# Kernel optimization log

Hardware: AMD Instinct MI355X
Metric: run time of the kernel (lower is better)

The kernel has to match this reference:

```python
import jax, jax.numpy as jnp
import numpy as np

N_SPOT, N_CITY, N_WORD = 20000, 2000, 20000
E_HAS, E_IN, E_DESC, E_RDESC = 100000, 100000, 400000, 400000
HID = 256


def setup_inputs() -> dict:
    key = jax.random.key(0)
    ks = jax.random.split(key, 48)

    def g(i, shape, s):
        return jax.random.normal(ks[i], shape, dtype=jnp.float32) * s

    inp = {}
    inp['x_spot'] = g(0, (N_SPOT, 2560), 0.5)
    inp['x_city'] = g(1, (N_CITY, 128), 0.5)
    inp['x_word'] = g(2, (N_WORD, 300), 0.5)
    inp['W_att'] = g(3, (4, 512, 128), 0.05)  # 4 heads, per_dim=128
    inp['q_att'] = g(4, (4, 128), 0.1)
    i = 5
    for n, d in [('w1_has_s', 128), ('w1_has_t', 512), ('w1_in_s', 512), ('w1_in_t', 128),
                 ('w1_desc_s', 300), ('w1_desc_t', 512), ('w1_rdesc_s', 512), ('w1_rdesc_t', 300)]:
        inp[n] = g(i, (d, HID), 0.05); i += 1
    for n in ['w2_has_s', 'w2_has_t', 'w2_in_s', 'w2_in_t', 'w2_desc_s', 'w2_desc_t', 'w2_rdesc_s', 'w2_rdesc_t']:
        inp[n] = g(i, (HID, HID), 0.05); i += 1
    for n in ['wl_spot', 'wl_city', 'wl_word']:
        inp[n] = g(i, (HID, 1), 0.05); i += 1
    for n in ['bl_spot', 'bl_city', 'bl_word']:
        inp[n] = jnp.zeros((1,), jnp.float32)
    for n, e, hi in [('e_has_src', E_HAS, N_CITY), ('e_has_tgt', E_HAS, N_SPOT),
                     ('e_in_src', E_IN, N_SPOT), ('e_in_tgt', E_IN, N_CITY),
                     ('e_desc_src', E_DESC, N_WORD), ('e_desc_tgt', E_DESC, N_SPOT),
                     ('e_rdesc_src', E_RDESC, N_SPOT), ('e_rdesc_tgt', E_RDESC, N_WORD)]:
        inp[n] = jax.random.randint(ks[i], (e,), 0, hi, dtype=jnp.int32); i += 1
    return inp


def _attention(x, W_att, q_att):
    # AttentionModule(input_dim=512, num_heads=4, split=5): (N, 2560) -> (N, 512)
    x = x.reshape(-1, 5, 512)
    xw = jnp.einsum('nsi,hio->hnso', x, W_att)                      # (4,N,5,128)
    a = jax.nn.leaky_relu(jnp.einsum('hnso,ho->hns', xw, q_att), 0.2)
    a = jax.nn.softmax(a, axis=2)                                   # softmax over split dim
    out = jnp.einsum('hnso,hns->hno', xw, a)                        # (4,N,128)
    return jnp.transpose(out, (1, 0, 2)).reshape(x.shape[0], 4 * 128)


def _scatter_mean(src, idx, n):
    s = jax.ops.segment_sum(src, idx, num_segments=n)
    c = jax.ops.segment_sum(jnp.ones((src.shape[0], 1), src.dtype), idx, num_segments=n)
    return s / jnp.maximum(c, 1.0)


def _edge(x_s, x_t, w_s, w_t, src, tgt):
    # per-edge-type linear, gather on source index, scatter-mean into targets
    msg = (x_s @ w_s)[src]
    return x_t @ w_t + _scatter_mean(msg, tgt, x_t.shape[0])


def _conv(xs, xc, xw, w, e):
    spot = _edge(xc, xs, w['has_s'], w['has_t'], e['has_src'], e['has_tgt']) \
         + _edge(xw, xs, w['desc_s'], w['desc_t'], e['desc_src'], e['desc_tgt'])
    city = _edge(xs, xc, w['in_s'], w['in_t'], e['in_src'], e['in_tgt'])
    word = _edge(xs, xw, w['rdesc_s'], w['rdesc_t'], e['rdesc_src'], e['rdesc_tgt'])
    # div[spot]=2, div[city]=div[word]=1; ReLU flag applies a second (idempotent) relu
    return jax.nn.relu(spot * 0.5), jax.nn.relu(city), jax.nn.relu(word)


def reference(x_spot, x_city, x_word, W_att, q_att,
              w1_has_s, w1_has_t, w1_in_s, w1_in_t, w1_desc_s, w1_desc_t, w1_rdesc_s, w1_rdesc_t,
              w2_has_s, w2_has_t, w2_in_s, w2_in_t, w2_desc_s, w2_desc_t, w2_rdesc_s, w2_rdesc_t,
              wl_spot, bl_spot, wl_city, bl_city, wl_word, bl_word,
              e_has_src, e_has_tgt, e_in_src, e_in_tgt, e_desc_src, e_desc_tgt, e_rdesc_src, e_rdesc_tgt):
    e = dict(has_src=e_has_src, has_tgt=e_has_tgt, in_src=e_in_src, in_tgt=e_in_tgt,
             desc_src=e_desc_src, desc_tgt=e_desc_tgt, rdesc_src=e_rdesc_src, rdesc_tgt=e_rdesc_tgt)
    w1 = dict(has_s=w1_has_s, has_t=w1_has_t, in_s=w1_in_s, in_t=w1_in_t,
              desc_s=w1_desc_s, desc_t=w1_desc_t, rdesc_s=w1_rdesc_s, rdesc_t=w1_rdesc_t)
    w2 = dict(has_s=w2_has_s, has_t=w2_has_t, in_s=w2_in_s, in_t=w2_in_t,
              desc_s=w2_desc_s, desc_t=w2_desc_t, rdesc_s=w2_rdesc_s, rdesc_t=w2_rdesc_t)
    xs = _attention(x_spot, W_att, q_att)  # multi=True path
    s1, c1, wd1 = _conv(xs, x_city, x_word, w1, e)
    s2, c2, wd2 = _conv(s1, c1, wd1, w2, e)
    out_spot = s2 @ wl_spot + bl_spot
    out_city = c2 @ wl_city + bl_city
    out_word = wd2 @ wl_word + bl_word
    # concat=True: mean over the two layer outputs per node type
    return ((s1 + s2) * 0.5, (c1 + c2) * 0.5, (wd1 + wd2) * 0.5, out_spot, out_city, out_word)
```

## Files before the change

### kernel.cpp

```cpp
#include <hip/hip_runtime.h>
#include <hip/hip_bf16.h>

#define HID 256
#define NSPOT 20000
#define NCITY 2000
#define NWORD 20000

typedef __attribute__((ext_vector_type(8))) short bhalf8;
typedef __attribute__((ext_vector_type(4))) float floatx4;

__device__ inline float bf2f(unsigned short u) {
    union { unsigned int i; float f; } v; v.i = (unsigned int)u << 16; return v.f;
}
__device__ inline unsigned short f2bf(float f) {
    __hip_bfloat16 b = __float2bfloat16(f);
    return *reinterpret_cast<unsigned short*>(&b);
}
__device__ inline float4 ld4(const float* p, size_t off) {
    return *reinterpret_cast<const float4*>(p + off);
}

__global__ void wq_kernel(const float* __restrict__ W, const float* __restrict__ q,
                          float* __restrict__ wq) {
    int idx = blockIdx.x * 256 + threadIdx.x;
// ... 36 lines not shown
            float v = al[tid][s];
            v = (v >= 0.f) ? v : 0.2f * v;
            z[s] = v; m = fmaxf(m, v);
        }
        float e[5]; float sum = 0.f;
        #pragma unroll
        for (int s = 0; s < 5; s++) { e[s] = __expf(z[s] - m); sum += e[s]; }
        float r = 1.f / sum;
        #pragma unroll
        for (int s = 0; s < 5; s++) al[tid][s] = e[s] * r;
    }
    __syncthreads();
    float a0 = al[wave][0], a1 = al[wave][1], a2 = al[wave][2], a3 = al[wave][3], a4 = al[wave][4];
    __hip_bfloat16* xo = xbar + ((size_t)wave * NSPOT + n) * 512;
    #pragma unroll
    for (int j = 0; j < 8; j++) {
        int i = lane + j * 64;
        float v = a0 * xl[i] + a1 * xl[512 + i] + a2 * xl[1024 + i] + a3 * xl[1536 + i] + a4 * xl[2048 + i];
        xo[i] = __float2bfloat16(v);
    }
}

#define KP 40
__global__ __launch_bounds__(256) void gemm_bf16(
    const __hip_bfloat16* __restrict__ A, int lda, long sA,
    const __hip_bfloat16* __restrict__ Bt, int ldb, long sB,
    float* __restrict__ C, int ldc,
    __hip_bfloat16* __restrict__ Cb, int ldcb, long sCb,
    int M, int N, int K) {
    __shared__ short As[128 * KP];
    __shared__ short Bs[128 * KP];
    int z = blockIdx.z;
    A += (size_t)z * sA;
    Bt += (size_t)z * sB;
    if (Cb) Cb += (size_t)z * sCb;
    int tid = threadIdx.x;
    int wave = tid >> 6, lane = tid & 63;
    int wr = wave & 1, wc = wave >> 1;
    int quad = lane >> 4, l16 = lane & 15;
    int rowbase = blockIdx.x * 128;
    int colbase = blockIdx.y * 128;
    int srow = tid >> 2;
    int skoff = (tid & 3) * 8;
    floatx4 acc[4][4];
    #pragma unroll
    for (int i = 0; i < 4; i++)
        #pragma unroll
        for (int j = 0; j < 4; j++)
            acc[i][j] = (floatx4){0.f, 0.f, 0.f, 0.f};

    for (int k0 = 0; k0 < K; k0 += 32) {
        #pragma unroll
        for (int i = 0; i < 2; i++) {
            int r = srow + i * 64;
            int gr = rowbase + r;
            int4 va = make_int4(0, 0, 0, 0);
            if (gr < M) va = *(const int4*)(A + (size_t)gr * lda + k0 + skoff);
            *(int4*)(As + r * KP + skoff) = va;
            int4 vb = *(const int4*)(Bt + (size_t)(colbase + r) * ldb + k0 + skoff);
            *(int4*)(Bs + r * KP + skoff) = vb;
        }
        __syncthreads();
        bhalf8 af[4], bfr[4];
        #pragma unroll
        for (int rt = 0; rt < 4; rt++)
            af[rt] = *(const bhalf8*)(As + (wr * 64 + rt * 16 + l16) * KP + quad * 8);
        #pragma unroll
        for (int ct = 0; ct < 4; ct++)
            bfr[ct] = *(const bhalf8*)(Bs + (wc * 64 + ct * 16 + l16) * KP + quad * 8);
        #pragma unroll
        for (int rt = 0; rt < 4; rt++)
            #pragma unroll
            for (int ct = 0; ct < 4; ct++)
                acc[rt][ct] = __builtin_amdgcn_mfma_f32_16x16x32_bf16(af[rt], bfr[ct], acc[rt][ct], 0, 0, 0);
        __syncthreads();
    }
    #pragma unroll
    for (int rt = 0; rt < 4; rt++) {
        #pragma unroll
        for (int r = 0; r < 4; r++) {
            int grow = rowbase + wr * 64 + rt * 16 + quad * 4 + r;
            if (grow < M) {
                #pragma unroll
                for (int ct = 0; ct < 4; ct++) {
                    int gcol = colbase + wc * 64 + ct * 16 + l16;
                    float v = acc[rt][ct][r];
                    if (C)  C[(size_t)grow * ldc + gcol] = v;
                    if (Cb) Cb[(size_t)grow * ldcb + gcol] = __float2bfloat16(v);
                }
            }
        }
    }
}

struct GemmDesc {
    const __hip_bfloat16* A;
    const __hip_bfloat16* Bt;
    float* C;
    __hip_bfloat16* Cb;
    int lda, ldb, ldc, ldcb, M, K;
};
struct GemmDesc8 { GemmDesc d[8]; };

__global__ __launch_bounds__(256) void gemm_bf16_grouped(GemmDesc8 descs) {
    GemmDesc g = descs.d[blockIdx.z];
    int rowbase = blockIdx.x * 128;
    if (rowbase >= g.M) return;
    __shared__ short As[128 * KP];
    __shared__ short Bs[128 * KP];
    int tid = threadIdx.x;
    int wave = tid >> 6, lane = tid & 63;
    int wr = wave & 1, wc = wave >> 1;
    int quad = lane >> 4, l16 = lane & 15;
    int colbase = blockIdx.y * 128;
    int srow = tid >> 2;
    int skoff = (tid & 3) * 8;
    floatx4 acc[4][4];
    #pragma unroll
    for (int i = 0; i < 4; i++)
        #pragma unroll
        for (int j = 0; j < 4; j++)
            acc[i][j] = (floatx4){0.f, 0.f, 0.f, 0.f};

    for (int k0 = 0; k0 < g.K; k0 += 32) {
        #pragma unroll
        for (int i = 0; i < 2; i++) {
            int r = srow + i * 64;
            int gr = rowbase + r;
            int4 va = make_int4(0, 0, 0, 0);
            if (gr < g.M) va = *(const int4*)(g.A + (size_t)gr * g.lda + k0 + skoff);
            *(int4*)(As + r * KP + skoff) = va;
            int4 vb = *(const int4*)(g.Bt + (size_t)(colbase + r) * g.ldb + k0 + skoff);
            *(int4*)(Bs + r * KP + skoff) = vb;
        }
        __syncthreads();
        bhalf8 af[4], bfr[4];
        #pragma unroll
        for (int rt = 0; rt < 4; rt++)
            af[rt] = *(const bhalf8*)(As + (wr * 64 + rt * 16 + l16) * KP + quad * 8);
        #pragma unroll
        for (int ct = 0; ct < 4; ct++)
            bfr[ct] = *(const bhalf8*)(Bs + (wc * 64 + ct * 16 + l16) * KP + quad * 8);
        #pragma unroll
        for (int rt = 0; rt < 4; rt++)
            #pragma unroll
            for (int ct = 0; ct < 4; ct++)
                acc[rt][ct] = __builtin_amdgcn_mfma_f32_16x16x32_bf16(af[rt], bfr[ct], acc[rt][ct], 0, 0, 0);
        __syncthreads();
    }
    #pragma unroll
    for (int rt = 0; rt < 4; rt++) {
        #pragma unroll
        for (int r = 0; r < 4; r++) {
            int grow = rowbase + wr * 64 + rt * 16 + quad * 4 + r;
            if (grow < g.M) {
                #pragma unroll
                for (int ct = 0; ct < 4; ct++) {
                    int gcol = colbase + wc * 64 + ct * 16 + l16;
                    float v = acc[rt][ct][r];
                    if (g.C)  g.C[(size_t)grow * g.ldc + gcol] = v;
                    if (g.Cb) g.Cb[(size_t)grow * g.ldcb + gcol] = __float2bfloat16(v);
                }
            }
        }
    }
}

struct TDesc { const float* in; __hip_bfloat16* out; int K; int N; int Kp; };
struct TDesc8 { TDesc d[8]; };
__global__ void transpose_cast_kernel(TDesc8 descs) {
    TDesc dsc = descs.d[blockIdx.z];
    __shared__ float tile[32][33];
    int k0 = blockIdx.x * 32, n0 = blockIdx.y * 32;
    if (k0 >= dsc.Kp || n0 >= dsc.N) return;
    int tn = threadIdx.x & 31, t8 = threadIdx.x >> 5;
    #pragma unroll
    for (int i = 0; i < 4; i++) {
        int k = k0 + t8 * 4 + i;
        float v = 0.f;
        if (k < dsc.K && n0 + tn < dsc.N) v = dsc.in[(size_t)k * dsc.N + n0 + tn];
        tile[t8 * 4 + i][tn] = v;
    }
    __syncthreads();
    int kk = threadIdx.x & 31, n8 = threadIdx.x >> 5;
    #pragma unroll
    for (int i = 0; i < 4; i++) {
        int n = n0 + n8 * 4 + i;
        int k = k0 + kk;
        if (n < dsc.N && k < dsc.Kp)
            dsc.out[(size_t)n * dsc.Kp + k] = __float2bfloat16(tile[kk][n8 * 4 + i]);
    }
}

__global__ void cast_kernel(const float* __restrict__ in, __hip_bfloat16* __restrict__ out, int n) {
    int i = blockIdx.x * 256 + threadIdx.x;
    if (i < n) out[i] = __float2bfloat16(in[i]);
}

__global__ void cast_pad_kernel(const float* __restrict__ in, __hip_bfloat16* __restrict__ out,
                                int rows, int K, int Kp) {
    int idx = blockIdx.x * 256 + threadIdx.x;
    if (idx >= rows * Kp) return;
    int r = idx / Kp, k = idx - r * Kp;
// ... 23 lines not shown
    for (int i = lo; i < hi; i++) s += dd.deg[i];
    part[tid] = s;
    __syncthreads();
    if (tid == 0) {
        int acc = 0;
        for (int i = 0; i < 256; i++) { partx[i] = acc; acc += part[i]; }
        partx[256] = acc;
    }
    __syncthreads();
    int acc = partx[tid];
    for (int i = lo; i < hi; i++) { dd.rp[i] = acc; dd.cur[i] = acc; acc += dd.deg[i]; }
    if (tid == 0) dd.rp[n] = partx[256];
}

__global__ void fill4_kernel(EdgeDesc4 ds) {
    EdgeDesc d = ds.d[blockIdx.y];
    int e = blockIdx.x * 256 + threadIdx.x;
    if (e >= d.E) return;
    int t = d.tgt[e];
    int pos = atomicAdd(&d.cur[t], 1);
    d.cs[pos] = d.src[e];
}

struct AggDesc { const __hip_bfloat16* msg; const int* rp; const int* cs; float* outm; };
struct AggDesc4 { AggDesc d[4]; int start1, start2, start3; };

__global__ __launch_bounds__(256) void agg4_kernel(AggDesc4 ds, int nrows) {
    int row = blockIdx.x * 4 + (threadIdx.x >> 6);
    if (row >= nrows) return;
    int lane = threadIdx.x & 63;
    int gi = (row >= ds.start1) + (row >= ds.start2) + (row >= ds.start3);
    int base = (gi == 0) ? 0 : (gi == 1) ? ds.start1 : (gi == 2) ? ds.start2 : ds.start3;
    AggDesc g = ds.d[gi];
    int t = row - base;
    int lo = g.rp[t], hi = g.rp[t + 1];
    float a0 = 0.f, a1 = 0.f, a2 = 0.f, a3 = 0.f;
    int doff = lane * 4;
    int i = lo;
    for (; i + 4 <= hi; i += 4) {
        int s0 = g.cs[i], s1 = g.cs[i + 1], s2 = g.cs[i + 2], s3 = g.cs[i + 3];
        ushort4 u0 = *(const ushort4*)(g.msg + (size_t)s0 * HID + doff);
        ushort4 u1 = *(const ushort4*)(g.msg + (size_t)s1 * HID + doff);
        ushort4 u2 = *(const ushort4*)(g.msg + (size_t)s2 * HID + doff);
        ushort4 u3 = *(const ushort4*)(g.msg + (size_t)s3 * HID + doff);
        a0 += (bf2f(u0.x) + bf2f(u1.x)) + (bf2f(u2.x) + bf2f(u3.x));
        a1 += (bf2f(u0.y) + bf2f(u1.y)) + (bf2f(u2.y) + bf2f(u3.y));
        a2 += (bf2f(u0.z) + bf2f(u1.z)) + (bf2f(u2.z) + bf2f(u3.z));
        a3 += (bf2f(u0.w) + bf2f(u1.w)) + (bf2f(u2.w) + bf2f(u3.w));
    }
    for (; i < hi; i++) {
        ushort4 u = *(const ushort4*)(g.msg + (size_t)g.cs[i] * HID + doff);
        a0 += bf2f(u.x); a1 += bf2f(u.y); a2 += bf2f(u.z); a3 += bf2f(u.w);
    }
    float inv = 1.f / fmaxf((float)(hi - lo), 1.f);
    float4 o = make_float4(a0 * inv, a1 * inv, a2 * inv, a3 * inv);
    *reinterpret_cast<float4*>(g.outm + (size_t)t * HID + doff) = o;
}

__global__ __launch_bounds__(256) void combine1v_kernel(
    const float* Sa, const float* Sb, const float* mH, const float* mD,
    float* s1, __hip_bfloat16* s1b,
    const float* Sc, const float* mI, float* c1, __hip_bfloat16* c1b,
    const float* Sw, const float* mR, float* wd1, __hip_bfloat16* wd1b) {
    int row = blockIdx.x * 4 + (threadIdx.x >> 6);
    if (row >= NSPOT + NCITY + NWORD) return;
    int lane = threadIdx.x & 63;
    float4 v; float* of; __hip_bfloat16* ob; size_t off;
    if (row < NSPOT) {
        off = (size_t)row * HID + lane * 4;
        float4 a = ld4(Sa, off), b = ld4(Sb, off), h = ld4(mH, off), d = ld4(mD, off);
        v = make_float4(fmaxf((a.x + b.x + h.x + d.x) * 0.5f, 0.f),
                        fmaxf((a.y + b.y + h.y + d.y) * 0.5f, 0.f),
                        fmaxf((a.z + b.z + h.z + d.z) * 0.5f, 0.f),
                        fmaxf((a.w + b.w + h.w + d.w) * 0.5f, 0.f));
        of = s1; ob = s1b;
    } else if (row < NSPOT + NCITY) {
        off = (size_t)(row - NSPOT) * HID + lane * 4;
        float4 a = ld4(Sc, off), m = ld4(mI, off);
        v = make_float4(fmaxf(a.x + m.x, 0.f), fmaxf(a.y + m.y, 0.f),
                        fmaxf(a.z + m.z, 0.f), fmaxf(a.w + m.w, 0.f));
        of = c1; ob = c1b;
    } else {
        off = (size_t)(row - NSPOT - NCITY) * HID + lane * 4;
        float4 a = ld4(Sw, off), m = ld4(mR, off);
        v = make_float4(fmaxf(a.x + m.x, 0.f), fmaxf(a.y + m.y, 0.f),
                        fmaxf(a.z + m.z, 0.f), fmaxf(a.w + m.w, 0.f));
        of = wd1; ob = wd1b;
    }
    *reinterpret_cast<float4*>(of + off) = v;
    ushort4 ub = make_ushort4(f2bf(v.x), f2bf(v.y), f2bf(v.z), f2bf(v.w));
    *reinterpret_cast<ushort4*>((unsigned short*)ob + off) = ub;
}

__global__ __launch_bounds__(256) void finale_kernel(
    const float* Sa, const float* Sb, const float* mH, const float* mD,
    const float* s1, float* out0, const float* wls, const float* bls, float* out3,
    const float* Sc, const float* mI, const float* c1, float* out1,
    const float* wlc, const float* blc, float* out4,
    const float* Sw, const float* mR, const float* wd1, float* out2,
    const float* wlw, const float* blw, float* out5) {
    int row = blockIdx.x * 4 + (threadIdx.x >> 6);
    if (row >= NSPOT + NCITY + NWORD) return;
    int lane = threadIdx.x & 63;
    float4 v, p; const float* wl; const float* bl; float* om; float* od;
    int r; size_t off;
    if (row < NSPOT) {
        r = row; off = (size_t)r * HID + lane * 4;
        float4 a = ld4(Sa, off), b = ld4(Sb, off), h = ld4(mH, off), d = ld4(mD, off);
        v = make_float4(fmaxf((a.x + b.x + h.x + d.x) * 0.5f, 0.f),
                        fmaxf((a.y + b.y + h.y + d.y) * 0.5f, 0.f),
                        fmaxf((a.z + b.z + h.z + d.z) * 0.5f, 0.f),
                        fmaxf((a.w + b.w + h.w + d.w) * 0.5f, 0.f));
        p = ld4(s1, off); wl = wls; bl = bls; om = out0; od = out3;
    } else if (row < NSPOT + NCITY) {
        r = row - NSPOT; off = (size_t)r * HID + lane * 4;
        float4 a = ld4(Sc, off), m = ld4(mI, off);
        v = make_float4(fmaxf(a.x + m.x, 0.f), fmaxf(a.y + m.y, 0.f),
                        fmaxf(a.z + m.z, 0.f), fmaxf(a.w + m.w, 0.f));
        p = ld4(c1, off); wl = wlc; bl = blc; om = out1; od = out4;
    } else {
        r = row - NSPOT - NCITY; off = (size_t)r * HID + lane * 4;
        float4 a = ld4(Sw, off), m = ld4(mR, off);
        v = make_float4(fmaxf(a.x + m.x, 0.f), fmaxf(a.y + m.y, 0.f),
                        fmaxf(a.z + m.z, 0.f), fmaxf(a.w + m.w, 0.f));
        p = ld4(wd1, off); wl = wlw; bl = blw; om = out2; od = out5;
    }
    float4 m4 = make_float4((p.x + v.x) * 0.5f, (p.y + v.y) * 0.5f,
                            (p.z + v.z) * 0.5f, (p.w + v.w) * 0.5f);
    *reinterpret_cast<float4*>(om + off) = m4;
    float4 w = *reinterpret_cast<const float4*>(wl + lane * 4);
    float s = v.x * w.x + v.y * w.y + v.z * w.z + v.w * w.w;
    #pragma unroll
    for (int o2 = 32; o2 > 0; o2 >>= 1) s += __shfl_down(s, o2, 64);
    if (lane == 0) od[r] = s + bl[0];
}

extern "C" void kernel_launch(void* const* d_in, const int* in_sizes, int n_in,
                              void* d_out, int out_size, void* d_ws, size_t ws_size,
                              hipStream_t stream) {
    const float* x_spot   = (const float*)d_in[0];
    const float* x_city   = (const float*)d_in[1];
    const float* x_word   = (const float*)d_in[2];
    const float* W_att    = (const float*)d_in[3];
    const float* q_att    = (const float*)d_in[4];
    const float* w1[8] = { (const float*)d_in[5], (const float*)d_in[6], (const float*)d_in[7],
                           (const float*)d_in[8], (const float*)d_in[9], (const float*)d_in[10],
                           (const float*)d_in[11], (const float*)d_in[12] };
    const float* w2[8] = { (const float*)d_in[13], (const float*)d_in[14], (const float*)d_in[15],
                           (const float*)d_in[16], (const float*)d_in[17], (const float*)d_in[18],
                           (const float*)d_in[19], (const float*)d_in[20] };
    const float* wl_spot = (const float*)d_in[21];
    const float* wl_city = (const float*)d_in[22];
    const float* wl_word = (const float*)d_in[23];
// ... 4 lines not shown
    const int* e_has_tgt   = (const int*)d_in[28];
    const int* e_in_src    = (const int*)d_in[29];
    const int* e_in_tgt    = (const int*)d_in[30];
    const int* e_desc_src  = (const int*)d_in[31];
    const int* e_desc_tgt  = (const int*)d_in[32];
    const int* e_rdesc_src = (const int*)d_in[33];
    const int* e_rdesc_tgt = (const int*)d_in[34];
    const int E_has   = in_sizes[27];
    const int E_in    = in_sizes[29];
    const int E_desc  = in_sizes[31];
    const int E_rdesc = in_sizes[33];

    float* out = (float*)d_out;
    float* wsf = (float*)d_ws;
    typedef __hip_bfloat16 bf;

    size_t o = 0;
    auto alloc = [&](size_t nfloats) { float* p = wsf + o; o += (nfloats + 15) & ~(size_t)15; return p; };
    float* wqb       = alloc(2048);
    bf* xs_bf        = (bf*)alloc((size_t)NSPOT * 512 / 2);
    bf* x_city_bf    = (bf*)alloc((size_t)NCITY * 128 / 2);
    bf* x_word_bf    = (bf*)alloc((size_t)NWORD * 320 / 2);
    bf* Wt_att       = (bf*)alloc((size_t)4 * 128 * 512 / 2);
    int K1[8]  = {128, 512, 512, 128, 300, 512, 512, 300};
    int Kp1[8] = {128, 512, 512, 128, 320, 512, 512, 320};
    bf* Wt1[8];
    for (int i = 0; i < 8; i++) Wt1[i] = (bf*)alloc((size_t)256 * Kp1[i] / 2);
    bf* Wt2[8];
    for (int i = 0; i < 8; i++) Wt2[i] = (bf*)alloc((size_t)256 * 256 / 2);
    float* Sa = alloc((size_t)NSPOT * HID);
    float* Sb = alloc((size_t)NSPOT * HID);
    float* Sc = alloc((size_t)NCITY * HID);
    float* Sw = alloc((size_t)NWORD * HID);
    float* m_has   = alloc((size_t)NSPOT * HID);
    float* m_desc  = alloc((size_t)NSPOT * HID);
    float* m_in    = alloc((size_t)NCITY * HID);
    float* m_rdesc = alloc((size_t)NWORD * HID);
    float* s1  = alloc((size_t)NSPOT * HID);
    float* c1  = alloc((size_t)NCITY * HID);
    float* wd1 = alloc((size_t)NWORD * HID);
    size_t regX = o;
    bf* xbar_bf = (bf*)(wsf + regX);
    size_t ox = regX;
    auto allocX = [&](size_t nfloats) { float* p = wsf + ox; ox += (nfloats + 15) & ~(size_t)15; return p; };
    bf* P_has_bf   = (bf*)allocX((size_t)NCITY * HID / 2);
    bf* P_in_bf    = (bf*)allocX((size_t)NSPOT * HID / 2);
    bf* P_desc_bf  = (bf*)allocX((size_t)NWORD * HID / 2);
    bf* P_rdesc_bf = (bf*)allocX((size_t)NSPOT * HID / 2);
    bf* s1b = (bf*)allocX((size_t)NSPOT * HID / 2);
    bf* c1b = (bf*)allocX((size_t)NCITY * HID / 2);
    bf* wd1b = (bf*)allocX((size_t)NWORD * HID / 2);
    o = regX + (size_t)4 * NSPOT * 512 / 2;
    int* wsi = (int*)(wsf + o);
    size_t io = 0;
    int* deg_has    = wsi + io; io += NSPOT;
    int* deg_desc   = wsi + io; io += NSPOT;
    int* deg_in     = wsi + io; io += NCITY;
    int* deg_rdesc  = wsi + io; io += NWORD;
    size_t deg_bytes = io * sizeof(int);
    int* rp_has     = wsi + io; io += NSPOT + 1;
    int* rp_desc    = wsi + io; io += NSPOT + 1;
    int* rp_in      = wsi + io; io += NCITY + 1;
    int* rp_rdesc   = wsi + io; io += NWORD + 1;
    int* cur_has    = wsi + io; io += NSPOT + 1;
    int* cur_desc   = wsi + io; io += NSPOT + 1;
    int* cur_in     = wsi + io; io += NCITY + 1;
    int* cur_rdesc  = wsi + io; io += NWORD + 1;
    int* cs_has     = wsi + io; io += E_has;
    int* cs_desc    = wsi + io; io += E_desc;
    int* cs_in      = wsi + io; io += E_in;
    int* cs_rdesc   = wsi + io; io += E_rdesc;
    (void)ws_size; (void)n_in; (void)out_size;

    {
        TDesc8 t{};
        for (int i = 0; i < 4; i++)
            t.d[i] = TDesc{ W_att + (size_t)i * 512 * 128, Wt_att + (size_t)i * 128 * 512, 512, 128, 512 };
        hipLaunchKernelGGL(transpose_cast_kernel, dim3(16, 4, 4), dim3(256), 0, stream, t);
    }
    {
        TDesc8 t{};
        for (int i = 0; i < 8; i++) t.d[i] = TDesc{ w1[i], Wt1[i], K1[i], 256, Kp1[i] };
        hipLaunchKernelGGL(transpose_cast_kernel, dim3(16, 8, 8), dim3(256), 0, stream, t);
    }
    {
        TDesc8 t{};
        for (int i = 0; i < 8; i++) t.d[i] = TDesc{ w2[i], Wt2[i], 256, 256, 256 };
        hipLaunchKernelGGL(transpose_cast_kernel, dim3(8, 8, 8), dim3(256), 0, stream, t);
    }
    hipLaunchKernelGGL(cast_kernel, dim3((NCITY * 128 + 255) / 256), dim3(256), 0, stream,
                       x_city, x_city_bf, NCITY * 128);
    hipLaunchKernelGGL(cast_pad_kernel, dim3((NWORD * 320 + 255) / 256), dim3(256), 0, stream,
                       x_word, x_word_bf, NWORD, 300, 320);

    EdgeDesc4 ed;
    ed.d[0] = EdgeDesc{ e_has_src,   e_has_tgt,   E_has,   NSPOT, deg_has,   rp_has,   cur_has,   cs_has };
    ed.d[1] = EdgeDesc{ e_desc_src,  e_desc_tgt,  E_desc,  NSPOT, deg_desc,  rp_desc,  cur_desc,  cs_desc };
    ed.d[2] = EdgeDesc{ e_in_src,    e_in_tgt,    E_in,    NCITY, deg_in,    rp_in,    cur_in,    cs_in };
    ed.d[3] = EdgeDesc{ e_rdesc_src, e_rdesc_tgt, E_rdesc, NWORD, deg_rdesc, rp_rdesc, cur_rdesc, cs_rdesc };
    int Emax = E_has;
    if (E_desc > Emax) Emax = E_desc;
    if (E_in > Emax) Emax = E_in;
    if (E_rdesc > Emax) Emax = E_rdesc;
    hipMemsetAsync((void*)deg_has, 0, deg_bytes, stream);
    hipLaunchKernelGGL(hist4_kernel, dim3((Emax + 255) / 256, 4), dim3(256), 0, stream, ed);
    hipLaunchKernelGGL(scan4_kernel, dim3(4), dim3(256), 0, stream, ed);
    hipLaunchKernelGGL(fill4_kernel, dim3((Emax + 255) / 256, 4), dim3(256), 0, stream, ed);

    hipLaunchKernelGGL(wq_kernel, dim3(8), dim3(256), 0, stream, W_att, q_att, wqb);
    hipLaunchKernelGGL(attn_kernel, dim3(NSPOT), dim3(256), 0, stream, x_spot, wqb, xbar_bf);
    {
        dim3 g((NSPOT + 127) / 128, 1, 4);
        hipLaunchKernelGGL(gemm_bf16, g, dim3(256), 0, stream,
                           xbar_bf, 512, (long)NSPOT * 512, Wt_att, 512, (long)128 * 512,
                           nullptr, 0, xs_bf, 512, 128, NSPOT, 128, 512);
    }

    int gx = (NSPOT + 127) / 128;

    {
        GemmDesc8 gd;
        gd.d[0] = GemmDesc{ x_city_bf, Wt1[0], nullptr, P_has_bf,   128, 128, 0, HID, NCITY, 128 };
        gd.d[1] = GemmDesc{ xs_bf,     Wt1[1], Sa,      nullptr,    512, 512, HID, 0, NSPOT, 512 };
        gd.d[2] = GemmDesc{ xs_bf,     Wt1[2], nullptr, P_in_bf,    512, 512, 0, HID, NSPOT, 512 };
        gd.d[3] = GemmDesc{ x_city_bf, Wt1[3], Sc,      nullptr,    128, 128, HID, 0, NCITY, 128 };
        gd.d[4] = GemmDesc{ x_word_bf, Wt1[4], nullptr, P_desc_bf,  320, 320, 0, HID, NWORD, 320 };
        gd.d[5] = GemmDesc{ xs_bf,     Wt1[5], Sb,      nullptr,    512, 512, HID, 0, NSPOT, 512 };
        gd.d[6] = GemmDesc{ xs_bf,     Wt1[6], nullptr, P_rdesc_bf, 512, 512, 0, HID, NSPOT, 512 };
        gd.d[7] = GemmDesc{ x_word_bf, Wt1[7], Sw,      nullptr,    320, 320, HID, 0, NWORD, 320 };
        hipLaunchKernelGGL(gemm_bf16_grouped, dim3(gx, 2, 8), dim3(256), 0, stream, gd);
    }

    AggDesc4 ag;
    ag.start1 = NSPOT; ag.start2 = 2 * NSPOT; ag.start3 = 2 * NSPOT + NCITY;
    int agg_rows = 2 * NSPOT + NCITY + NWORD;
    ag.d[0] = AggDesc{ P_has_bf,   rp_has,   cs_has,   m_has };
    ag.d[1] = AggDesc{ P_desc_bf,  rp_desc,  cs_desc,  m_desc };
    ag.d[2] = AggDesc{ P_in_bf,    rp_in,    cs_in,    m_in };
    ag.d[3] = AggDesc{ P_rdesc_bf, rp_rdesc, cs_rdesc, m_rdesc };
    hipLaunchKernelGGL(agg4_kernel, dim3((agg_rows + 3) / 4), dim3(256), 0, stream, ag, agg_rows);
    hipLaunchKernelGGL(combine1v_kernel, dim3((NSPOT + NCITY + NWORD) / 4), dim3(256), 0, stream,
                       Sa, Sb, m_has, m_desc, s1, s1b,
                       Sc, m_in, c1, c1b,
                       Sw, m_rdesc, wd1, wd1b);

    {
        GemmDesc8 gd;
        gd.d[0] = GemmDesc{ c1b,  Wt2[0], nullptr, P_has_bf,   HID, HID, 0, HID, NCITY, HID };
        gd.d[1] = GemmDesc{ s1b,  Wt2[1], Sa,      nullptr,    HID, HID, HID, 0, NSPOT, HID };
        gd.d[2] = GemmDesc{ s1b,  Wt2[2], nullptr, P_in_bf,    HID, HID, 0, HID, NSPOT, HID };
        gd.d[3] = GemmDesc{ c1b,  Wt2[3], Sc,      nullptr,    HID, HID, HID, 0, NCITY, HID };
        gd.d[4] = GemmDesc{ wd1b, Wt2[4], nullptr, P_desc_bf,  HID, HID, 0, HID, NWORD, HID };
        gd.d[5] = GemmDesc{ s1b,  Wt2[5], Sb,      nullptr,    HID, HID, HID, 0, NSPOT, HID };
        gd.d[6] = GemmDesc{ s1b,  Wt2[6], nullptr, P_rdesc_bf, HID, HID, 0, HID, NSPOT, HID };
        gd.d[7] = GemmDesc{ wd1b, Wt2[7], Sw,      nullptr,    HID, HID, HID, 0, NWORD, HID };
        hipLaunchKernelGGL(gemm_bf16_grouped, dim3(gx, 2, 8), dim3(256), 0, stream, gd);
    }

    hipLaunchKernelGGL(agg4_kernel, dim3((agg_rows + 3) / 4), dim3(256), 0, stream, ag, agg_rows);

    float* out0 = out;
    float* out1 = out + (size_t)NSPOT * HID;
    float* out2 = out1 + (size_t)NCITY * HID;
    float* out3 = out2 + (size_t)NWORD * HID;
    float* out4 = out3 + NSPOT;
    float* out5 = out4 + NCITY;
    hipLaunchKernelGGL(finale_kernel, dim3((NSPOT + NCITY + NWORD) / 4), dim3(256), 0, stream,
                       Sa, Sb, m_has, m_desc, s1, out0, wl_spot, bl_spot, out3,
                       Sc, m_in, c1, out1, wl_city, bl_city, out4,
                       Sw, m_rdesc, wd1, out2, wl_word, bl_word, out5);
}
```

Baseline: 960.8 us.

## Fuse segment-mean aggregation into combine kernels and merge shared spot self-weights

Removes the separate agg4 kernel and its fp32 mean buffers by computing segment means inline in the combine and finale kernels. The two spot-target self-transform weights (has_t and desc_t) are pre-summed during transpose, so one GEMM writes a single Ss instead of Sa and Sb. The attention GEMM is expressed through the grouped kernel, which gains an N bound check. This cuts fp32 intermediate traffic and one GEMM per layer. The fused kernels do more gather work per row, and pre-summing the weights before the bf16 cast changes rounding slightly.

```diff
diff --git a/kernel.cpp b/kernel.cpp
--- a/kernel.cpp
+++ b/kernel.cpp
@@ -82,26 +82,31 @@
 }
 
 #define KP 40
-__global__ __launch_bounds__(256) void gemm_bf16(
-    const __hip_bfloat16* __restrict__ A, int lda, long sA,
-    const __hip_bfloat16* __restrict__ Bt, int ldb, long sB,
-    float* __restrict__ C, int ldc,
-    __hip_bfloat16* __restrict__ Cb, int ldcb, long sCb,
-    int M, int N, int K) {
+struct GemmDesc {
+    const __hip_bfloat16* A;
+    const __hip_bfloat16* Bt;
+    float* C;
+    __hip_bfloat16* Cb;
+    int lda, ldb, ldc, ldcb, M, K, N;
+};
+struct GemmDesc8 { GemmDesc d[8]; };
+
+__global__ __launch_bounds__(256) void gemm_grouped(GemmDesc8 descs) {
+    GemmDesc g = descs.d[blockIdx.z];
+    int rowbase = blockIdx.x * 128;
+    int colbase = blockIdx.y * 128;
+    if (rowbase >= g.M || colbase >= g.N) return;
     __shared__ short As[128 * KP];
     __shared__ short Bs[128 * KP];
-    int z = blockIdx.z;
-    A += (size_t)z * sA;
-    Bt += (size_t)z * sB;
-    if (Cb) Cb += (size_t)z * sCb;
     int tid = threadIdx.x;
     int wave = tid >> 6, lane = tid & 63;
     int wr = wave & 1, wc = wave >> 1;
     int quad = lane >> 4, l16 = lane & 15;
-    int rowbase = blockIdx.x * 128;
-    int colbase = blockIdx.y * 128;
     int srow = tid >> 2;
     int skoff = (tid & 3) * 8;
+    const __hip_bfloat16* A = g.A;
+    const __hip_bfloat16* Bt = g.Bt;
+    int lda = g.lda, ldb = g.ldb, M = g.M, K = g.K;
     floatx4 acc[4][4];
     #pragma unroll
     for (int i = 0; i < 4; i++)
@@ -145,79 +150,6 @@
                 for (int ct = 0; ct < 4; ct++) {
                     int gcol = colbase + wc * 64 + ct * 16 + l16;
                     float v = acc[rt][ct][r];
-                    if (C)  C[(size_t)grow * ldc + gcol] = v;
-                    if (Cb) Cb[(size_t)grow * ldcb + gcol] = __float2bfloat16(v);
-                }
-            }
-        }
-    }
-}
-
-struct GemmDesc {
-    const __hip_bfloat16* A;
-    const __hip_bfloat16* Bt;
-    float* C;
-    __hip_bfloat16* Cb;
-    int lda, ldb, ldc, ldcb, M, K;
-};
-struct GemmDesc8 { GemmDesc d[8]; };
-
-__global__ __launch_bounds__(256) void gemm_bf16_grouped(GemmDesc8 descs) {
-    GemmDesc g = descs.d[blockIdx.z];
-    int rowbase = blockIdx.x * 128;
-    if (rowbase >= g.M) return;
-    __shared__ short As[128 * KP];
-    __shared__ short Bs[128 * KP];
-    int tid = threadIdx.x;
-    int wave = tid >> 6, lane = tid & 63;
-    int wr = wave & 1, wc = wave >> 1;
-    int quad = lane >> 4, l16 = lane & 15;
-    int colbase = blockIdx.y * 128;
-    int srow = tid >> 2;
-    int skoff = (tid & 3) * 8;
-    floatx4 acc[4][4];
-    #pragma unroll
-    for (int i = 0; i < 4; i++)
-        #pragma unroll
-        for (int j = 0; j < 4; j++)
-            acc[i][j] = (floatx4){0.f, 0.f, 0.f, 0.f};
-
-    for (int k0 = 0; k0 < g.K; k0 += 32) {
-        #pragma unroll
-        for (int i = 0; i < 2; i++) {
-            int r = srow + i * 64;
-            int gr = rowbase + r;
-            int4 va = make_int4(0, 0, 0, 0);
-            if (gr < g.M) va = *(const int4*)(g.A + (size_t)gr * g.lda + k0 + skoff);
-            *(int4*)(As + r * KP + skoff) = va;
-            int4 vb = *(const int4*)(g.Bt + (size_t)(colbase + r) * g.ldb + k0 + skoff);
-            *(int4*)(Bs + r * KP + skoff) = vb;
-        }
-        __syncthreads();
-        bhalf8 af[4], bfr[4];
-        #pragma unroll
-        for (int rt = 0; rt < 4; rt++)
-            af[rt] = *(const bhalf8*)(As + (wr * 64 + rt * 16 + l16) * KP + quad * 8);
-        #pragma unroll
-        for (int ct = 0; ct < 4; ct++)
-            bfr[ct] = *(const bhalf8*)(Bs + (wc * 64 + ct * 16 + l16) * KP + quad * 8);
-        #pragma unroll
-        for (int rt = 0; rt < 4; rt++)
-            #pragma unroll
-            for (int ct = 0; ct < 4; ct++)
-                acc[rt][ct] = __builtin_amdgcn_mfma_f32_16x16x32_bf16(af[rt], bfr[ct], acc[rt][ct], 0, 0, 0);
-        __syncthreads();
-    }
-    #pragma unroll
-    for (int rt = 0; rt < 4; rt++) {
-        #pragma unroll
-        for (int r = 0; r < 4; r++) {
-            int grow = rowbase + wr * 64 + rt * 16 + quad * 4 + r;
-            if (grow < g.M) {
-                #pragma unroll
-                for (int ct = 0; ct < 4; ct++) {
-                    int gcol = colbase + wc * 64 + ct * 16 + l16;
-                    float v = acc[rt][ct][r];
                     if (g.C)  g.C[(size_t)grow * g.ldc + gcol] = v;
                     if (g.Cb) g.Cb[(size_t)grow * g.ldcb + gcol] = __float2bfloat16(v);
                 }
@@ -226,7 +158,7 @@
     }
 }
 
-struct TDesc { const float* in; __hip_bfloat16* out; int K; int N; int Kp; };
+struct TDesc { const float* in; const float* in2; __hip_bfloat16* out; int K; int N; int Kp; };
 struct TDesc8 { TDesc d[8]; };
 __global__ void transpose_cast_kernel(TDesc8 descs) {
     TDesc dsc = descs.d[blockIdx.z];
@@ -238,7 +170,10 @@
     for (int i = 0; i < 4; i++) {
         int k = k0 + t8 * 4 + i;
         float v = 0.f;
-        if (k < dsc.K && n0 + tn < dsc.N) v = dsc.in[(size_t)k * dsc.N + n0 + tn];
+        if (k < dsc.K && n0 + tn < dsc.N) {
+            v = dsc.in[(size_t)k * dsc.N + n0 + tn];
+            if (dsc.in2) v += dsc.in2[(size_t)k * dsc.N + n0 + tn];
+        }
         tile[t8 * 4 + i][tn] = v;
     }
     __syncthreads();
@@ -308,69 +243,70 @@
     d.cs[pos] = d.src[e];
 }
 
-struct AggDesc { const __hip_bfloat16* msg; const int* rp; const int* cs; float* outm; };
-struct AggDesc4 { AggDesc d[4]; int start1, start2, start3; };
-
-__global__ __launch_bounds__(256) void agg4_kernel(AggDesc4 ds, int nrows) {
-    int row = blockIdx.x * 4 + (threadIdx.x >> 6);
-    if (row >= nrows) return;
-    int lane = threadIdx.x & 63;
-    int gi = (row >= ds.start1) + (row >= ds.start2) + (row >= ds.start3);
-    int base = (gi == 0) ? 0 : (gi == 1) ? ds.start1 : (gi == 2) ? ds.start2 : ds.start3;
-    AggDesc g = ds.d[gi];
-    int t = row - base;
-    int lo = g.rp[t], hi = g.rp[t + 1];
+__device__ inline float4 seg_mean(const __hip_bfloat16* __restrict__ msg,
+                                  const int* __restrict__ rp, const int* __restrict__ cs,
+                                  int t, int doff) {
+    int lo = rp[t], hi = rp[t + 1];
     float a0 = 0.f, a1 = 0.f, a2 = 0.f, a3 = 0.f;
-    int doff = lane * 4;
     int i = lo;
     for (; i + 4 <= hi; i += 4) {
-        int s0 = g.cs[i], s1 = g.cs[i + 1], s2 = g.cs[i + 2], s3 = g.cs[i + 3];
-        ushort4 u0 = *(const ushort4*)(g.msg + (size_t)s0 * HID + doff);
-        ushort4 u1 = *(const ushort4*)(g.msg + (size_t)s1 * HID + doff);
-        ushort4 u2 = *(const ushort4*)(g.msg + (size_t)s2 * HID + doff);
-        ushort4 u3 = *(const ushort4*)(g.msg + (size_t)s3 * HID + doff);
+        int s0 = cs[i], s1 = cs[i + 1], s2 = cs[i + 2], s3 = cs[i + 3];
+        ushort4 u0 = *(const ushort4*)(msg + (size_t)s0 * HID + doff);
+        ushort4 u1 = *(const ushort4*)(msg + (size_t)s1 * HID + doff);
+        ushort4 u2 = *(const ushort4*)(msg + (size_t)s2 * HID + doff);
+        ushort4 u3 = *(const ushort4*)(msg + (size_t)s3 * HID + doff);
         a0 += (bf2f(u0.x) + bf2f(u1.x)) + (bf2f(u2.x) + bf2f(u3.x));
         a1 += (bf2f(u0.y) + bf2f(u1.y)) + (bf2f(u2.y) + bf2f(u3.y));
         a2 += (bf2f(u0.z) + bf2f(u1.z)) + (bf2f(u2.z) + bf2f(u3.z));
         a3 += (bf2f(u0.w) + bf2f(u1.w)) + (bf2f(u2.w) + bf2f(u3.w));
     }
     for (; i < hi; i++) {
-        ushort4 u = *(const ushort4*)(g.msg + (size_t)g.cs[i] * HID + doff);
+        ushort4 u = *(const ushort4*)(msg + (size_t)cs[i] * HID + doff);
         a0 += bf2f(u.x); a1 += bf2f(u.y); a2 += bf2f(u.z); a3 += bf2f(u.w);
     }
     float inv = 1.f / fmaxf((float)(hi - lo), 1.f);
-    float4 o = make_float4(a0 * inv, a1 * inv, a2 * inv, a3 * inv);
-    *reinterpret_cast<float4*>(g.outm + (size_t)t * HID + doff) = o;
-}
-
-__global__ __launch_bounds__(256) void combine1v_kernel(
-    const float* Sa, const float* Sb, const float* mH, const float* mD,
-    float* s1, __hip_bfloat16* s1b,
-    const float* Sc, const float* mI, float* c1, __hip_bfloat16* c1b,
-    const float* Sw, const float* mR, float* wd1, __hip_bfloat16* wd1b) {
+    return make_float4(a0 * inv, a1 * inv, a2 * inv, a3 * inv);
+}
+
+__global__ __launch_bounds__(256) void fused_ac1_kernel(
+    const __hip_bfloat16* __restrict__ Phas,   const int* __restrict__ rp_has,   const int* __restrict__ cs_has,
+    const __hip_bfloat16* __restrict__ Pdesc,  const int* __restrict__ rp_desc,  const int* __restrict__ cs_desc,
+    const __hip_bfloat16* __restrict__ Pin,    const int* __restrict__ rp_in,    const int* __restrict__ cs_in,
+    const __hip_bfloat16* __restrict__ Prdesc, const int* __restrict__ rp_rdesc, const int* __restrict__ cs_rdesc,
+    const float* __restrict__ Ss, const float* __restrict__ Sc, const float* __restrict__ Sw,
+    float* __restrict__ s1, __hip_bfloat16* __restrict__ s1b,
+    float* __restrict__ c1, __hip_bfloat16* __restrict__ c1b,
+    float* __restrict__ wd1, __hip_bfloat16* __restrict__ wd1b) {
     int row = blockIdx.x * 4 + (threadIdx.x >> 6);
     if (row >= NSPOT + NCITY + NWORD) return;
     int lane = threadIdx.x & 63;
+    int doff = lane * 4;
     float4 v; float* of; __hip_bfloat16* ob; size_t off;
     if (row < NSPOT) {
-        off = (size_t)row * HID + lane * 4;
-        float4 a = ld4(Sa, off), b = ld4(Sb, off), h = ld4(mH, off), d = ld4(mD, off);
-        v = make_float4(fmaxf((a.x + b.x + h.x + d.x) * 0.5f, 0.f),
-                        fmaxf((a.y + b.y + h.y + d.y) * 0.5f, 0.f),
-                        fmaxf((a.z + b.z + h.z + d.z) * 0.5f, 0.f),
-                        fmaxf((a.w + b.w + h.w + d.w) * 0.5f, 0.f));
+        float4 mh = seg_mean(Phas, rp_has, cs_has, row, doff);
+        float4 md = seg_mean(Pdesc, rp_desc, cs_desc, row, doff);
+        off = (size_t)row * HID + doff;
+        float4 s = ld4(Ss, off);
+        v = make_float4(fmaxf((s.x + mh.x + md.x) * 0.5f, 0.f),
+                        fmaxf((s.y + mh.y + md.y) * 0.5f, 0.f),
+                        fmaxf((s.z + mh.z + md.z) * 0.5f, 0.f),
+                        fmaxf((s.w + mh.w + md.w) * 0.5f, 0.f));
         of = s1; ob = s1b;
     } else if (row < NSPOT + NCITY) {
-        off = (size_t)(row - NSPOT) * HID + lane * 4;
-        float4 a = ld4(Sc, off), m = ld4(mI, off);
-        v = make_float4(fmaxf(a.x + m.x, 0.f), fmaxf(a.y + m.y, 0.f),
-                        fmaxf(a.z + m.z, 0.f), fmaxf(a.w + m.w, 0.f));
+        int r = row - NSPOT;
+        float4 mi = seg_mean(Pin, rp_in, cs_in, r, doff);
+        off = (size_t)r * HID + doff;
+        float4 s = ld4(Sc, off);
+        v = make_float4(fmaxf(s.x + mi.x, 0.f), fmaxf(s.y + mi.y, 0.f),
+                        fmaxf(s.z + mi.z, 0.f), fmaxf(s.w + mi.w, 0.f));
         of = c1; ob = c1b;
     } else {
-        off = (size_t)(row - NSPOT - NCITY) * HID + lane * 4;
-        float4 a = ld4(Sw, off), m = ld4(mR, off);
-        v = make_float4(fmaxf(a.x + m.x, 0.f), fmaxf(a.y + m.y, 0.f),
-                        fmaxf(a.z + m.z, 0.f), fmaxf(a.w + m.w, 0.f));
+        int r = row - NSPOT - NCITY;
+        float4 mr = seg_mean(Prdesc, rp_rdesc, cs_rdesc, r, doff);
+        off = (size_t)r * HID + doff;
+        float4 s = ld4(Sw, off);
+        v = make_float4(fmaxf(s.x + mr.x, 0.f), fmaxf(s.y + mr.y, 0.f),
+                        fmaxf(s.z + mr.z, 0.f), fmaxf(s.w + mr.w, 0.f));
         of = wd1; ob = wd1b;
     }
     *reinterpret_cast<float4*>(of + off) = v;
@@ -378,43 +314,54 @@
     *reinterpret_cast<ushort4*>((unsigned short*)ob + off) = ub;
 }
 
-__global__ __launch_bounds__(256) void finale_kernel(
-    const float* Sa, const float* Sb, const float* mH, const float* mD,
-    const float* s1, float* out0, const float* wls, const float* bls, float* out3,
-    const float* Sc, const float* mI, const float* c1, float* out1,
-    const float* wlc, const float* blc, float* out4,
-    const float* Sw, const float* mR, const float* wd1, float* out2,
-    const float* wlw, const float* blw, float* out5) {
+__global__ __launch_bounds__(256) void fused_finale_kernel(
+    const __hip_bfloat16* __restrict__ Phas,   const int* __restrict__ rp_has,   const int* __restrict__ cs_has,
+    const __hip_bfloat16* __restrict__ Pdesc,  const int* __restrict__ rp_desc,  const int* __restrict__ cs_desc,
+    const __hip_bfloat16* __restrict__ Pin,    const int* __restrict__ rp_in,    const int* __restrict__ cs_in,
+    const __hip_bfloat16* __restrict__ Prdesc, const int* __restrict__ rp_rdesc, const int* __restrict__ cs_rdesc,
+    const float* __restrict__ Ss, const float* __restrict__ Sc, const float* __restrict__ Sw,
+    const float* __restrict__ s1, const float* __restrict__ c1, const float* __restrict__ wd1,
+    float* __restrict__ out0, const float* __restrict__ wls, const float* __restrict__ bls, float* __restrict__ out3,
+    float* __restrict__ out1, const float* __restrict__ wlc, const float* __restrict__ blc, float* __restrict__ out4,
+    float* __restrict__ out2, const float* __restrict__ wlw, const float* __restrict__ blw, float* __restrict__ out5) {
     int row = blockIdx.x * 4 + (threadIdx.x >> 6);
     if (row >= NSPOT + NCITY + NWORD) return;
     int lane = threadIdx.x & 63;
+    int doff = lane * 4;
     float4 v, p; const float* wl; const float* bl; float* om; float* od;
     int r; size_t off;
     if (row < NSPOT) {
-        r = row; off = (size_t)r * HID + lane * 4;
-        float4 a = ld4(Sa, off), b = ld4(Sb, off), h = ld4(mH, off), d = ld4(mD, off);
-        v = make_float4(fmaxf((a.x + b.x + h.x + d.x) * 0.5f, 0.f),
-                        fmaxf((a.y + b.y + h.y + d.y) * 0.5f, 0.f),
-                        fmaxf((a.z + b.z + h.z + d.z) * 0.5f, 0.f),
-                        fmaxf((a.w + b.w + h.w + d.w) * 0.5f, 0.f));
+        r = row;
+        float4 mh = seg_mean(Phas, rp_has, cs_has, r, doff);
+        float4 md = seg_mean(Pdesc, rp_desc, cs_desc, r, doff);
+        off = (size_t)r * HID + doff;
+        float4 s = ld4(Ss, off);
+        v = make_float4(fmaxf((s.x + mh.x + md.x) * 0.5f, 0.f),
+                        fmaxf((s.y + mh.y + md.y) * 0.5f, 0.f),
+                        fmaxf((s.z + mh.z + md.z) * 0.5f, 0.f),
+                        fmaxf((s.w + mh.w + md.w) * 0.5f, 0.f));
         p = ld4(s1, off); wl = wls; bl = bls; om = out0; od = out3;
     } else if (row < NSPOT + NCITY) {
-        r = row - NSPOT; off = (size_t)r * HID + lane * 4;
-        float4 a = ld4(Sc, off), m = ld4(mI, off);
-        v = make_float4(fmaxf(a.x + m.x, 0.f), fmaxf(a.y + m.y, 0.f),
-                        fmaxf(a.z + m.z, 0.f), fmaxf(a.w + m.w, 0.f));
+        r = row - NSPOT;
+        float4 mi = seg_mean(Pin, rp_in, cs_in, r, doff);
+        off = (size_t)r * HID + doff;
+        float4 s = ld4(Sc, off);
+        v = make_float4(fmaxf(s.x + mi.x, 0.f), fmaxf(s.y + mi.y, 0.f),
+                        fmaxf(s.z + mi.z, 0.f), fmaxf(s.w + mi.w, 0.f));
         p = ld4(c1, off); wl = wlc; bl = blc; om = out1; od = out4;
     } else {
-        r = row - NSPOT - NCITY; off = (size_t)r * HID + lane * 4;
-        float4 a = ld4(Sw, off), m = ld4(mR, off);
-        v = make_float4(fmaxf(a.x + m.x, 0.f), fmaxf(a.y + m.y, 0.f),
-                        fmaxf(a.z + m.z, 0.f), fmaxf(a.w + m.w, 0.f));
+        r = row - NSPOT - NCITY;
+        float4 mr = seg_mean(Prdesc, rp_rdesc, cs_rdesc, r, doff);
+        off = (size_t)r * HID + doff;
+        float4 s = ld4(Sw, off);
+        v = make_float4(fmaxf(s.x + mr.x, 0.f), fmaxf(s.y + mr.y, 0.f),
+                        fmaxf(s.z + mr.z, 0.f), fmaxf(s.w + mr.w, 0.f));
         p = ld4(wd1, off); wl = wlw; bl = blw; om = out2; od = out5;
     }
     float4 m4 = make_float4((p.x + v.x) * 0.5f, (p.y + v.y) * 0.5f,
                             (p.z + v.z) * 0.5f, (p.w + v.w) * 0.5f);
     *reinterpret_cast<float4*>(om + off) = m4;
-    float4 w = *reinterpret_cast<const float4*>(wl + lane * 4);
+    float4 w = *reinterpret_cast<const float4*>(wl + doff);
     float s = v.x * w.x + v.y * w.y + v.z * w.z + v.w * w.w;
     #pragma unroll
     for (int o2 = 32; o2 > 0; o2 >>= 1) s += __shfl_down(s, o2, 64);
@@ -465,20 +412,14 @@
     bf* x_city_bf    = (bf*)alloc((size_t)NCITY * 128 / 2);
     bf* x_word_bf    = (bf*)alloc((size_t)NWORD * 320 / 2);
     bf* Wt_att       = (bf*)alloc((size_t)4 * 128 * 512 / 2);
-    int K1[8]  = {128, 512, 512, 128, 300, 512, 512, 300};
-    int Kp1[8] = {128, 512, 512, 128, 320, 512, 512, 320};
-    bf* Wt1[8];
-    for (int i = 0; i < 8; i++) Wt1[i] = (bf*)alloc((size_t)256 * Kp1[i] / 2);
-    bf* Wt2[8];
-    for (int i = 0; i < 8; i++) Wt2[i] = (bf*)alloc((size_t)256 * 256 / 2);
-    float* Sa = alloc((size_t)NSPOT * HID);
-    float* Sb = alloc((size_t)NSPOT * HID);
+    int Kp1[7] = {128, 512, 512, 128, 320, 512, 320};
+    bf* Wt1[7];
+    for (int i = 0; i < 7; i++) Wt1[i] = (bf*)alloc((size_t)256 * Kp1[i] / 2);
+    bf* Wt2[7];
+    for (int i = 0; i < 7; i++) Wt2[i] = (bf*)alloc((size_t)256 * 256 / 2);
+    float* Ss = alloc((size_t)NSPOT * HID);
     float* Sc = alloc((size_t)NCITY * HID);
     float* Sw = alloc((size_t)NWORD * HID);
-    float* m_has   = alloc((size_t)NSPOT * HID);
-    float* m_desc  = alloc((size_t)NSPOT * HID);
-    float* m_in    = alloc((size_t)NCITY * HID);
-    float* m_rdesc = alloc((size_t)NWORD * HID);
     float* s1  = alloc((size_t)NSPOT * HID);
     float* c1  = alloc((size_t)NCITY * HID);
     float* wd1 = alloc((size_t)NWORD * HID);
@@ -518,17 +459,30 @@
     {
         TDesc8 t{};
         for (int i = 0; i < 4; i++)
-            t.d[i] = TDesc{ W_att + (size_t)i * 512 * 128, Wt_att + (size_t)i * 128 * 512, 512, 128, 512 };
+            t.d[i] = TDesc{ W_att + (size_t)i * 512 * 128, nullptr,
+                            Wt_att + (size_t)i * 128 * 512, 512, 128, 512 };
         hipLaunchKernelGGL(transpose_cast_kernel, dim3(16, 4, 4), dim3(256), 0, stream, t);
     }
     {
         TDesc8 t{};
-        for (int i = 0; i < 8; i++) t.d[i] = TDesc{ w1[i], Wt1[i], K1[i], 256, Kp1[i] };
+        t.d[0] = TDesc{ w1[0], nullptr, Wt1[0], 128, 256, 128 };
+        t.d[1] = TDesc{ w1[1], w1[5],   Wt1[1], 512, 256, 512 };
+        t.d[2] = TDesc{ w1[2], nullptr, Wt1[2], 512, 256, 512 };
+        t.d[3] = TDesc{ w1[3], nullptr, Wt1[3], 128, 256, 128 };
+        t.d[4] = TDesc{ w1[4], nullptr, Wt1[4], 300, 256, 320 };
+        t.d[5] = TDesc{ w1[6], nullptr, Wt1[5], 512, 256, 512 };
+        t.d[6] = TDesc{ w1[7], nullptr, Wt1[6], 300, 256, 320 };
         hipLaunchKernelGGL(transpose_cast_kernel, dim3(16, 8, 8), dim3(256), 0, stream, t);
     }
     {
         TDesc8 t{};
-        for (int i = 0; i < 8; i++) t.d[i] = TDesc{ w2[i], Wt2[i], 256, 256, 256 };
+        t.d[0] = TDesc{ w2[0], nullptr, Wt2[0], 256, 256, 256 };
+        t.d[1] = TDesc{ w2[1], w2[5],   Wt2[1], 256, 256, 256 };
+        t.d[2] = TDesc{ w2[2], nullptr, Wt2[2], 256, 256, 256 };
+        t.d[3] = TDesc{ w2[3], nullptr, Wt2[3], 256, 256, 256 };
+        t.d[4] = TDesc{ w2[4], nullptr, Wt2[4], 256, 256, 256 };
+        t.d[5] = TDesc{ w2[6], nullptr, Wt2[5], 256, 256, 256 };
+        t.d[6] = TDesc{ w2[7], nullptr, Wt2[6], 256, 256, 256 };
         hipLaunchKernelGGL(transpose_cast_kernel, dim3(8, 8, 8), dim3(256), 0, stream, t);
     }
     hipLaunchKernelGGL(cast_kernel, dim3((NCITY * 128 + 255) / 256), dim3(256), 0, stream,
@@ -552,55 +506,48 @@
 
     hipLaunchKernelGGL(wq_kernel, dim3(8), dim3(256), 0, stream, W_att, q_att, wqb);
     hipLaunchKernelGGL(attn_kernel, dim3(NSPOT), dim3(256), 0, stream, x_spot, wqb, xbar_bf);
+
+    int gx = (NSPOT + 127) / 128;
+
     {
-        dim3 g((NSPOT + 127) / 128, 1, 4);
-        hipLaunchKernelGGL(gemm_bf16, g, dim3(256), 0, stream,
-                           xbar_bf, 512, (long)NSPOT * 512, Wt_att, 512, (long)128 * 512,
-                           nullptr, 0, xs_bf, 512, 128, NSPOT, 128, 512);
-    }
-
-    int gx = (NSPOT + 127) / 128;
+        GemmDesc8 gd{};
+        for (int h = 0; h < 4; h++)
+            gd.d[h] = GemmDesc{ xbar_bf + (size_t)h * NSPOT * 512, Wt_att + (size_t)h * 128 * 512,
+                                nullptr, xs_bf + h * 128, 512, 512, 0, 512, NSPOT, 512, 128 };
+        hipLaunchKernelGGL(gemm_grouped, dim3(gx, 1, 4), dim3(256), 0, stream, gd);
+    }
 
     {
-        GemmDesc8 gd;
-        gd.d[0] = GemmDesc{ x_city_bf, Wt1[0], nullptr, P_has_bf,   128, 128, 0, HID, NCITY, 128 };
-        gd.d[1] = GemmDesc{ xs_bf,     Wt1[1], Sa,      nullptr,    512, 512, HID, 0, NSPOT, 512 };
-        gd.d[2] = GemmDesc{ xs_bf,     Wt1[2], nullptr, P_in_bf,    512, 512, 0, HID, NSPOT, 512 };
-        gd.d[3] = GemmDesc{ x_city_bf, Wt1[3], Sc,      nullptr,    128, 128, HID, 0, NCITY, 128 };
-        gd.d[4] = GemmDesc{ x_word_bf, Wt1[4], nullptr, P_desc_bf,  320, 320, 0, HID, NWORD, 320 };
-        gd.d[5] = GemmDesc{ xs_bf,     Wt1[5], Sb,      nullptr,    512, 512, HID, 0, NSPOT, 512 };
-        gd.d[6] = GemmDesc{ xs_bf,     Wt1[6], nullptr, P_rdesc_bf, 512, 512, 0, HID, NSPOT, 512 };
-        gd.d[7] = GemmDesc{ x_word_bf, Wt1[7], Sw,      nullptr,    320, 320, HID, 0, NWORD, 320 };
-        hipLaunchKernelGGL(gemm_bf16_grouped, dim3(gx, 2, 8), dim3(256), 0, stream, gd);
-    }
-
-    AggDesc4 ag;
-    ag.start1 = NSPOT; ag.start2 = 2 * NSPOT; ag.start3 = 2 * NSPOT + NCITY;
-    int agg_rows = 2 * NSPOT + NCITY + NWORD;
-    ag.d[0] = AggDesc{ P_has_bf,   rp_has,   cs_has,   m_has };
-    ag.d[1] = AggDesc{ P_desc_bf,  rp_desc,  cs_desc,  m_desc };
-    ag.d[2] = AggDesc{ P_in_bf,    rp_in,    cs_in,    m_in };
-    ag.d[3] = AggDesc{ P_rdesc_bf, rp_rdesc, cs_rdesc, m_rdesc };
-    hipLaunchKernelGGL(agg4_kernel, dim3((agg_rows + 3) / 4), dim3(256), 0, stream, ag, agg_rows);
-    hipLaunchKernelGGL(combine1v_kernel, dim3((NSPOT + NCITY + NWORD) / 4), dim3(256), 0, stream,
-                       Sa, Sb, m_has, m_desc, s1, s1b,
-                       Sc, m_in, c1, c1b,
-                       Sw, m_rdesc, wd1, wd1b);
+        GemmDesc8 gd{};
+        gd.d[0] = GemmDesc{ x_city_bf, Wt1[0], nullptr, P_has_bf,   128, 128, 0, HID, NCITY, 128, HID };
+        gd.d[1] = GemmDesc{ xs_bf,     Wt1[1], Ss,      nullptr,    512, 512, HID, 0, NSPOT, 512, HID };
+        gd.d[2] = GemmDesc{ xs_bf,     Wt1[2], nullptr, P_in_bf,    512, 512, 0, HID, NSPOT, 512, HID };
+        gd.d[3] = GemmDesc{ x_city_bf, Wt1[3], Sc,      nullptr,    128, 128, HID, 0, NCITY, 128, HID };
+        gd.d[4] = GemmDesc{ x_word_bf, Wt1[4], nullptr, P_desc_bf,  320, 320, 0, HID, NWORD, 320, HID };
+        gd.d[5] = GemmDesc{ xs_bf,     Wt1[5], nullptr, P_rdesc_bf, 512, 512, 0, HID, NSPOT, 512, HID };
+        gd.d[6] = GemmDesc{ x_word_bf, Wt1[6], Sw,      nullptr,    320, 320, HID, 0, NWORD, 320, HID };
+        gd.d[7].M = 0; gd.d[7].N = 0;
+        hipLaunchKernelGGL(gemm_grouped, dim3(gx, 2, 8), dim3(256), 0, stream, gd);
+    }
+
+    int rows3 = NSPOT + NCITY + NWORD;
+    hipLaunchKernelGGL(fused_ac1_kernel, dim3((rows3 + 3) / 4), dim3(256), 0, stream,
+                       P_has_bf, rp_has, cs_has, P_desc_bf, rp_desc, cs_desc,
+                       P_in_bf, rp_in, cs_in, P_rdesc_bf, rp_rdesc, cs_rdesc,
+                       Ss, Sc, Sw, s1, s1b, c1, c1b, wd1, wd1b);
 
     {
-        GemmDesc8 gd;
-        gd.d[0] = GemmDesc{ c1b,  Wt2[0], nullptr, P_has_bf,   HID, HID, 0, HID, NCITY, HID };
-        gd.d[1] = GemmDesc{ s1b,  Wt2[1], Sa,      nullptr,    HID, HID, HID, 0, NSPOT, HID };
-        gd.d[2] = GemmDesc{ s1b,  Wt2[2], nullptr, P_in_bf,    HID, HID, 0, HID, NSPOT, HID };
-        gd.d[3] = GemmDesc{ c1b,  Wt2[3], Sc,      nullptr,    HID, HID, HID, 0, NCITY, HID };
-        gd.d[4] = GemmDesc{ wd1b, Wt2[4], nullptr, P_desc_bf,  HID, HID, 0, HID, NWORD, HID };
-        gd.d[5] = GemmDesc{ s1b,  Wt2[5], Sb,      nullptr,    HID, HID, HID, 0, NSPOT, HID };
-        gd.d[6] = GemmDesc{ s1b,  Wt2[6], nullptr, P_rdesc_bf, HID, HID, 0, HID, NSPOT, HID };
-        gd.d[7] = GemmDesc{ wd1b, Wt2[7], Sw,      nullptr,    HID, HID, HID, 0, NWORD, HID };
-        hipLaunchKernelGGL(gemm_bf16_grouped, dim3(gx, 2, 8), dim3(256), 0, stream, gd);
-    }
-
-    hipLaunchKernelGGL(agg4_kernel, dim3((agg_rows + 3) / 4), dim3(256), 0, stream, ag, agg_rows);
+        GemmDesc8 gd{};
+        gd.d[0] = GemmDesc{ c1b,  Wt2[0], nullptr, P_has_bf,   HID, HID, 0, HID, NCITY, HID, HID };
+        gd.d[1] = GemmDesc{ s1b,  Wt2[1], Ss,      nullptr,    HID, HID, HID, 0, NSPOT, HID, HID };
+        gd.d[2] = GemmDesc{ s1b,  Wt2[2], nullptr, P_in_bf,    HID, HID, 0, HID, NSPOT, HID, HID };
+        gd.d[3] = GemmDesc{ c1b,  Wt2[3], Sc,      nullptr,    HID, HID, HID, 0, NCITY, HID, HID };
+        gd.d[4] = GemmDesc{ wd1b, Wt2[4], nullptr, P_desc_bf,  HID, HID, 0, HID, NWORD, HID, HID };
+        gd.d[5] = GemmDesc{ s1b,  Wt2[5], nullptr, P_rdesc_bf, HID, HID, 0, HID, NSPOT, HID, HID };
+        gd.d[6] = GemmDesc{ wd1b, Wt2[6], Sw,      nullptr,    HID, HID, HID, 0, NWORD, HID, HID };
+        gd.d[7].M = 0; gd.d[7].N = 0;
+        hipLaunchKernelGGL(gemm_grouped, dim3(gx, 2, 8), dim3(256), 0, stream, gd);
+    }
 
     float* out0 = out;
     float* out1 = out + (size_t)NSPOT * HID;
@@ -608,8 +555,11 @@
     float* out3 = out2 + (size_t)NWORD * HID;
     float* out4 = out3 + NSPOT;
     float* out5 = out4 + NCITY;
-    hipLaunchKernelGGL(finale_kernel, dim3((NSPOT + NCITY + NWORD) / 4), dim3(256), 0, stream,
-                       Sa, Sb, m_has, m_desc, s1, out0, wl_spot, bl_spot, out3,
-                       Sc, m_in, c1, out1, wl_city, bl_city, out4,
-                       Sw, m_rdesc, wd1, out2, wl_word, bl_word, out5);
-}
+    hipLaunchKernelGGL(fused_finale_kernel, dim3((rows3 + 3) / 4), dim3(256), 0, stream,
+                       P_has_bf, rp_has, cs_has, P_desc_bf, rp_desc, cs_desc,
+                       P_in_bf, rp_in, cs_in, P_rdesc_bf, rp_rdesc, cs_rdesc,
+                       Ss, Sc, Sw, s1, c1, wd1,
+                       out0, wl_spot, bl_spot, out3,
+                       out1, wl_city, bl_city, out4,
+                       out2, wl_word, bl_word, out5);
+}
```

Result: faster. 842.7 us (-12.3%).
